# Kernel tuning notes

Hardware: AMD Instinct MI355X
Metric: run time of the kernel (lower is better)

## Reference

```python
import math
import jax, jax.numpy as jnp
import numpy as np

B, T, HIDDEN = 2, 2048, 1024
H, HKV, D = 16, 16, 64


def _rope_tables(T, D):
    inv_freq = 1.0 / (10000.0 ** (jnp.arange(0, D, 2, dtype=jnp.float32) / D))
    t = jnp.arange(T, dtype=jnp.float32)
    freqs = jnp.outer(t, inv_freq)               # [T, D/2]
    emb = jnp.concatenate([freqs, freqs], axis=-1)  # [T, D]
    return jnp.cos(emb), jnp.sin(emb)


def setup_inputs() -> dict:
    key = jax.random.key(0)
    k1, k2, k3 = jax.random.split(key, 3)
    hidden_states = jax.random.normal(k1, (B, T, HIDDEN), dtype=jnp.float32)
    cos, sin = _rope_tables(T, D)
    # trunc-normal-ish init, std = 1/sqrt(fan_in)
    w_qkv = jax.random.normal(k2, ((H + 2 * HKV) * D, HIDDEN), dtype=jnp.float32) / math.sqrt(HIDDEN)
    w_o = jax.random.normal(k3, (HIDDEN, H * D), dtype=jnp.float32) / math.sqrt(H * D)
    return {"hidden_states": hidden_states, "cos": cos, "sin": sin, "w_qkv": w_qkv, "w_o": w_o}


def _rotate_half(x):
    x1, x2 = jnp.split(x, 2, axis=-1)
    return jnp.concatenate([-x2, x1], axis=-1)


def reference(hidden_states, cos, sin, w_qkv, w_o):
    b, t, _ = hidden_states.shape
    # fused QKV projection: [B,T,(H+2*HKV)*D]
    qkv = jnp.einsum('bti,oi->bto', hidden_states, w_qkv)
    qkv = qkv.reshape(b, t, H + 2 * HKV, D)
    q = qkv[:, :, :H]                    # [B,T,H,D]
    k = qkv[:, :, H:H + HKV]             # [B,T,HKV,D]
    v = qkv[:, :, H + HKV:]              # [B,T,HKV,D]
    # inline RoPE; cos/sin broadcast over heads
    c = cos[:, None, :]
    s = sin[:, None, :]
    q = q * c + _rotate_half(q) * s
    k = k * c + _rotate_half(k) * s
    scale = 1.0 / math.sqrt(D)
    attn_scores = jnp.einsum('bthd,bThd->bhtT', q, k) * scale  # [B,H,T,T]
    mask = jnp.tril(jnp.ones((t, t), dtype=bool))
    attn_scores = jnp.where(mask[None, None, :, :], attn_scores, -1e9)
    attn = jax.nn.softmax(attn_scores, axis=-1)
    context = jnp.einsum('bhtT,bThd->bthd', attn, v).reshape(b, t, H * D)
    return jnp.einsum('bti,oi->bto', context, w_o)
```

## Files before the change

### kernel.cpp

```cpp
#include <hip/hip_runtime.h>

typedef __bf16 bf16_t;
typedef __bf16 bf16x4 __attribute__((ext_vector_type(4)));
typedef __bf16 bf16x8 __attribute__((ext_vector_type(8)));
typedef float f32x4 __attribute__((ext_vector_type(4)));
typedef unsigned int u32x2 __attribute__((ext_vector_type(2)));
typedef unsigned long long u64;

#define MFMA16(a, b, c) __builtin_amdgcn_mfma_f32_16x16x32_bf16((a), (b), (c), 0, 0, 0)

#define LDG2LDS16(g, l)                                                        \
    __builtin_amdgcn_global_load_lds(                                          \
        (const __attribute__((address_space(1))) void*)(g),                    \
        (__attribute__((address_space(3))) void*)(l), 16, 0, 0)

#if __has_builtin(__builtin_amdgcn_exp2f)
#define EXP2(x) __builtin_amdgcn_exp2f(x)
#else
#define EXP2(x) exp2f(x)
#endif

__device__ inline bf16x8 load8(const float* p) {
    const f32x4 a = *(const f32x4*)p;
    const f32x4 b = *(const f32x4*)(p + 4);
    bf16x8 r;
#pragma unroll
    for (int i = 0; i < 4; i++) { r[i] = (bf16_t)a[i]; r[4 + i] = (bf16_t)b[i]; }
    return r;
}

__device__ inline u32x2 as2(bf16x4 v) {
    u32x2 r;
    __builtin_memcpy(&r, &v, 8);
    return r;
}

__device__ inline bf16x4 shfl4(bf16x4 v, int src) {
    u64 x;
    __builtin_memcpy(&x, &v, 8);
    x = __shfl(x, src, 64);
    bf16x4 r;
    __builtin_memcpy(&r, &x, 8);
    return r;
}

__global__ __launch_bounds__(256) void convert_kernel(const float* __restrict__ hs,
                                                      const float* __restrict__ wqkv,
                                                      const float* __restrict__ wo,
                                                      bf16_t* __restrict__ outb) {
    const size_t c = ((size_t)blockIdx.x * 256 + threadIdx.x) * 8;
    const float* src;
    size_t off;
    if (c < 4194304) { src = hs; off = c; }
    else if (c < 7340032) { src = wqkv; off = c - 4194304; }
    else { src = wo; off = c - 7340032; }
    *(bf16x8*)(outb + c) = load8(src + off);
}


__global__ __launch_bounds__(512, 2) void gemm_qkv256(const bf16_t* __restrict__ A,
                                                      const bf16_t* __restrict__ B,
                                                      bf16_t* __restrict__ q_ws,
                                                      bf16_t* __restrict__ k_ws,
                                                      bf16_t* __restrict__ v_ws,
                                                      const float* __restrict__ cosb,
                                                      const float* __restrict__ sinb) {
    constexpr int K = 1024;
    __shared__ __align__(16) bf16_t As[32768];
    __shared__ __align__(16) bf16_t Bs[32768];

    const int tid = threadIdx.x;
    const int w = tid >> 6;
    const int lane = tid & 63;
    const int lr = lane & 15;
    const int quad = lane >> 4;

    const int lid = blockIdx.x;
    const int l = (lid & 7) * 24 + (lid >> 3);
    const int by = l / 12;
    const int bx = l - by * 12;
    const int m0 = by * 256;
    const int n0 = bx * 256;

    const int trow = tid >> 3;
    const int slot = (tid & 7) ^ (trow & 7);
    const bf16_t* gA = A + (size_t)(m0 + trow) * K + slot * 8;
    const bf16_t* gB = B + (size_t)(n0 + trow) * K + slot * 8;
    bf16_t* lA = As + w * 512;
    bf16_t* lB = Bs + w * 512;

    const int wmm = (w >> 2) * 128;
    const int wnn = (w & 3) * 64;
    const int offA0 = (quad ^ (lr & 7)) * 16;
    const char* Ab = (const char*)As + (wmm + lr) * 128;
    const char* Bb = (const char*)Bs + (wnn + lr) * 128;

    f32x4 acc[8][4] = {};

#define STAGE256(t, buf)                                                       \
    {                                                                          \
        _Pragma("unroll") for (int c = 0; c < 4; c++) {                        \
            LDG2LDS16(gA + (size_t)c * 65536 + (size_t)(t) * 64,               \
                      lA + (buf) * 16384 + c * 4096);                          \
            LDG2LDS16(gB + (size_t)c * 65536 + (size_t)(t) * 64,               \
                      lB + (buf) * 16384 + c * 4096);                          \
        }                                                                      \
    }

#define PHASE256(buf, qm, qn)                                                  \
    {                                                                          \
        const char* pa = Ab + (buf) * 32768 + (qm) * 8192;                     \
        const char* pb = Bb + (buf) * 32768 + (qn) * 4096;                     \
        {                                                                      \
            bf16x8 a0[4], b0[2];                                               \
            _Pragma("unroll") for (int i = 0; i < 4; i++)                      \
                a0[i] = *(const bf16x8*)(pa + i * 2048 + offA0);               \
            _Pragma("unroll") for (int jn = 0; jn < 2; jn++)                   \
                b0[jn] = *(const bf16x8*)(pb + jn * 2048 + offA0);             \
            __builtin_amdgcn_s_setprio(1);                                     \
            _Pragma("unroll") for (int i = 0; i < 4; i++)                      \
                _Pragma("unroll") for (int jn = 0; jn < 2; jn++)               \
                    acc[(qm) * 4 + i][(qn) * 2 + jn] = MFMA16(                 \
                        a0[i], b0[jn], acc[(qm) * 4 + i][(qn) * 2 + jn]);      \
            __builtin_amdgcn_s_setprio(0);                                     \
        }                                                                      \
        {                                                                      \
            bf16x8 a1[4], b1[2];                                               \
            _Pragma("unroll") for (int i = 0; i < 4; i++)                      \
                a1[i] = *(const bf16x8*)(pa + i * 2048 + (offA0 ^ 64));        \
            _Pragma("unroll") for (int jn = 0; jn < 2; jn++)                   \
                b1[jn] = *(const bf16x8*)(pb + jn * 2048 + (offA0 ^ 64));      \
            __builtin_amdgcn_s_setprio(1);                                     \
            _Pragma("unroll") for (int i = 0; i < 4; i++)                      \
                _Pragma("unroll") for (int jn = 0; jn < 2; jn++)               \
                    acc[(qm) * 4 + i][(qn) * 2 + jn] = MFMA16(                 \
                        a1[i], b1[jn], acc[(qm) * 4 + i][(qn) * 2 + jn]);      \
            __builtin_amdgcn_s_setprio(0);                                     \
        }                                                                      \
    }

    STAGE256(0, 0);
    STAGE256(1, 1);
    asm volatile("s_waitcnt vmcnt(8)" ::: "memory");
    __builtin_amdgcn_s_barrier();
    asm volatile("" ::: "memory");

#pragma unroll 2
    for (int t = 0; t < 16; t++) {
        const int buf = t & 1;
        PHASE256(buf, 0, 0);
        PHASE256(buf, 0, 1);
        PHASE256(buf, 1, 0);
        PHASE256(buf, 1, 1);
        asm volatile("s_waitcnt lgkmcnt(0)" ::: "memory");
        __builtin_amdgcn_s_barrier();
        asm volatile("" ::: "memory");
        if (t < 14) {
            STAGE256(t + 2, buf);
            asm volatile("s_waitcnt vmcnt(8)" ::: "memory");
        } else {
            asm volatile("s_waitcnt vmcnt(0)" ::: "memory");
        }
        __builtin_amdgcn_s_barrier();
        asm volatile("" ::: "memory");
    }

#undef STAGE256
#undef PHASE256

    const int j = bx * 4 + (w & 3);
    if (j < 32) {
        const bool isq = (j < 16);
        const float qs = 0.125f * 1.44269504089f;
#pragma unroll
        for (int im = 0; im < 8; im++) {
#pragma unroll
            for (int r = 0; r < 4; r++) {
                const int m = m0 + wmm + im * 16 + quad * 4 + r;
                const int b = m >> 11;
                const int t = m & 2047;
#pragma unroll
                for (int in = 0; in < 2; in++) {
                    const int d = in * 16 + lr;
                    const float x1 = acc[im][in][r];
                    const float x2 = acc[im][in + 2][r];
                    const float c = cosb[t * 64 + d];
                    const float s = sinb[t * 64 + d];
                    float y1 = x1 * c - x2 * s;
                    float y2 = x2 * c + x1 * s;
                    if (isq) {
                        y1 *= qs; y2 *= qs;
                        const size_t base =
                            ((size_t)(b * 16 + j) * 2048 + t) * 64 + d;
                        q_ws[base] = (bf16_t)y1;
                        q_ws[base + 32] = (bf16_t)y2;
                    } else {
                        const int bh = b * 16 + (j - 16);
                        const size_t off =
                            ((size_t)(bh * 128 + (t >> 4)) * 2) * 512 +
                            ((t & 15) + (d >> 3) * 16) * 8 + (d & 7);
                        k_ws[off] = (bf16_t)y1;
                        k_ws[off + 512] = (bf16_t)y2;
                    }
                }
            }
        }
    } else {
#pragma unroll
        for (int im = 0; im < 8; im++)
#pragma unroll
            for (int in = 0; in < 4; in++)
#pragma unroll
                for (int r = 0; r < 4; r++) {
                    const int m = m0 + wmm + im * 16 + quad * 4 + r;
                    const int b = m >> 11;
                    const int t = m & 2047;
                    const int d = in * 16 + lr;
                    const int bh = b * 16 + (j - 32);
                    const size_t off =
                        ((size_t)(bh * 64 + (t >> 5)) * 4 + (d >> 4)) * 512 +
                        ((d & 15) + ((t & 31) >> 3) * 16) * 8 + (t & 7);
                    v_ws[off] = (bf16_t)acc[im][in][r];
                }
    }
}

template <int MODE, int NDIM, int BM>
__global__ __launch_bounds__(256) void gemm_bt(const bf16_t* __restrict__ A,
                                               const bf16_t* __restrict__ B,
                                               float* __restrict__ outp,
                                               bf16_t* __restrict__ q_ws,
                                               bf16_t* __restrict__ k_ws,
                                               bf16_t* __restrict__ v_ws,
                                               const float* __restrict__ cosb,
                                               const float* __restrict__ sinb) {
    constexpr int K = 1024;
    constexpr int IM = BM / 32;
    __shared__ __align__(16) bf16_t As[BM * 32];
    __shared__ __align__(16) bf16_t Bs[128 * 32];

    const int tid = threadIdx.x;
    const int w = tid >> 6;
    const int lane = tid & 63;
    const int lr = lane & 15;
    const int quad = lane >> 4;
    const int m0 = blockIdx.y * BM;
    const int n0 = blockIdx.x * 128;
    const int wm = (w & 1) * (BM / 2);
    const int wn = (w >> 1) * 64;

    const int srow = tid >> 2;
    const int skk = (tid & 3) * 8;
    const bf16_t* gA0 = A + (size_t)(m0 + srow) * K + skk;
    const bf16_t* gA1 = gA0 + (size_t)64 * K;
    const bf16_t* gB0 = B + (size_t)(n0 + srow) * K + skk;
    const bf16_t* gB1 = gB0 + (size_t)64 * K;
    bf16_t* lA0 = As + w * 512;
    bf16_t* lA1 = As + 2048 + w * 512;
    bf16_t* lB0 = Bs + w * 512;
    bf16_t* lB1 = Bs + 2048 + w * 512;

    f32x4 acc[IM][4] = {};

    for (int k0 = 0; k0 < K; k0 += 32) {
        LDG2LDS16(gA0 + k0, lA0);
        if constexpr (BM == 128) LDG2LDS16(gA1 + k0, lA1);
        LDG2LDS16(gB0 + k0, lB0);
        LDG2LDS16(gB1 + k0, lB1);
        __syncthreads();

        bf16x8 af[IM], bfm[4];
#pragma unroll
        for (int im = 0; im < IM; im++)
            af[im] = *(const bf16x8*)&As[(wm + im * 16 + lr) * 32 + quad * 8];
#pragma unroll
        for (int in = 0; in < 4; in++)
            bfm[in] = *(const bf16x8*)&Bs[(wn + in * 16 + lr) * 32 + quad * 8];
#pragma unroll
        for (int im = 0; im < IM; im++)
#pragma unroll
            for (int in = 0; in < 4; in++)
                acc[im][in] = MFMA16(af[im], bfm[in], acc[im][in]);
        __syncthreads();
    }

    if constexpr (MODE == 0) {
#pragma unroll
        for (int im = 0; im < IM; im++)
#pragma unroll
            for (int in = 0; in < 4; in++)
#pragma unroll
                for (int r = 0; r < 4; r++) {
                    const int m = m0 + wm + im * 16 + quad * 4 + r;
                    const int n = n0 + wn + in * 16 + lr;
                    outp[(size_t)m * NDIM + n] = acc[im][in][r];
                }
    } else {
        const int j = (n0 + wn) >> 6;
        if (j < 32) {
            const bool isq = (j < 16);
            const float qs = 0.125f * 1.44269504089f;
#pragma unroll
            for (int im = 0; im < IM; im++) {
#pragma unroll
                for (int r = 0; r < 4; r++) {
                    const int m = m0 + wm + im * 16 + quad * 4 + r;
                    const int b = m >> 11;
                    const int t = m & 2047;
#pragma unroll
                    for (int in = 0; in < 2; in++) {
                        const int d = in * 16 + lr;
                        const float x1 = acc[im][in][r];
                        const float x2 = acc[im][in + 2][r];
                        const float c = cosb[t * 64 + d];
                        const float s = sinb[t * 64 + d];
                        float y1 = x1 * c - x2 * s;
                        float y2 = x2 * c + x1 * s;
                        if (isq) {
                            y1 *= qs; y2 *= qs;
                            const size_t base =
                                ((size_t)(b * 16 + j) * 2048 + t) * 64 + d;
                            q_ws[base] = (bf16_t)y1;
                            q_ws[base + 32] = (bf16_t)y2;
                        } else {
                            const int bh = b * 16 + (j - 16);
                            const size_t off =
                                ((size_t)(bh * 128 + (t >> 4)) * 2) * 512 +
                                ((t & 15) + (d >> 3) * 16) * 8 + (d & 7);
                            k_ws[off] = (bf16_t)y1;
                            k_ws[off + 512] = (bf16_t)y2;
                        }
                    }
                }
            }
        } else {
#pragma unroll
            for (int im = 0; im < IM; im++)
#pragma unroll
                for (int in = 0; in < 4; in++)
#pragma unroll
                    for (int r = 0; r < 4; r++) {
                        const int m = m0 + wm + im * 16 + quad * 4 + r;
                        const int b = m >> 11;
                        const int t = m & 2047;
                        const int d = in * 16 + lr;
                        const int bh = b * 16 + (j - 32);
                        const size_t off =
                            ((size_t)(bh * 64 + (t >> 5)) * 4 + (d >> 4)) * 512 +
                            ((d & 15) + ((t & 31) >> 3) * 16) * 8 + (t & 7);
                        v_ws[off] = (bf16_t)acc[im][in][r];
                    }
        }
    }
}

__device__ inline void flash_tile(int qt, int quad, int lr, int query,
                                  const bf16_t* __restrict__ kbase,
                                  const bf16_t* __restrict__ vbase,
                                  bf16x8 qlo, bf16x8 qhi,
                                  f32x4* o, float& lrun) {
    bf16x8 kc[8];
#pragma unroll
    for (int n = 0; n < 4; n++) {
        kc[2 * n] = *(const bf16x8*)(kbase + (size_t)(n * 2) * 512);
        kc[2 * n + 1] = *(const bf16x8*)(kbase + (size_t)(n * 2 + 1) * 512);
    }

    for (int kb = 0; kb <= qt; kb++) {
        bf16x8 vv[2][4];
#pragma unroll
        for (int hh = 0; hh < 2; hh++)
#pragma unroll
            for (int n = 0; n < 4; n++)
                vv[hh][n] = *(const bf16x8*)(vbase +
                    (size_t)((kb * 2 + hh) * 4 + n) * 512);

        const int kbn = (kb < qt) ? kb + 1 : kb;
        bf16x8 kn[8];
#pragma unroll
        for (int n = 0; n < 4; n++) {
            kn[2 * n] = *(const bf16x8*)(kbase + (size_t)((kbn * 4 + n) * 2) * 512);
            kn[2 * n + 1] = *(const bf16x8*)(kbase + (size_t)((kbn * 4 + n) * 2 + 1) * 512);
        }

        const int u0 = kb * 64;
        f32x4 s[4];
#pragma unroll
        for (int n = 0; n < 4; n++) {
            const f32x4 z = {};
            s[n] = MFMA16(kc[2 * n], qlo, z);
            s[n] = MFMA16(kc[2 * n + 1], qhi, s[n]);
        }

        if (kb == qt) {
#pragma unroll
            for (int n = 0; n < 4; n++)
#pragma unroll
                for (int r = 0; r < 4; r++)
                    if (u0 + n * 16 + quad * 4 + r > query) s[n][r] = -1e9f;
        }

        f32x4 p[4];
#pragma unroll
        for (int n = 0; n < 4; n++)
#pragma unroll
            for (int r = 0; r < 4; r++) p[n][r] = EXP2(s[n][r]);

        lrun += ((p[0][0] + p[0][1]) + (p[0][2] + p[0][3])) +
                ((p[1][0] + p[1][1]) + (p[1][2] + p[1][3])) +
                ((p[2][0] + p[2][1]) + (p[2][2] + p[2][3])) +
                ((p[3][0] + p[3][1]) + (p[3][2] + p[3][3]));

        bf16x4 pb[4];
#pragma unroll
        for (int n = 0; n < 4; n++)
#pragma unroll
            for (int r = 0; r < 4; r++) pb[n][r] = (bf16_t)p[n][r];

#pragma unroll
        for (int hh = 0; hh < 2; hh++) {
            bf16x8 pf;
#if __has_builtin(__builtin_amdgcn_permlane16_swap) && \
    __has_builtin(__builtin_amdgcn_permlane32_swap)
            const u32x2 P0 = as2(pb[2 * hh]);
            const u32x2 P1 = as2(pb[2 * hh + 1]);
            const u32x2 s1a = __builtin_amdgcn_permlane16_swap(P0[0], P0[1], false, false);
            const u32x2 s1b = __builtin_amdgcn_permlane16_swap(P1[0], P1[1], false, false);
            const u32x2 s2a = __builtin_amdgcn_permlane32_swap(s1a[0], s1b[0], false, false);
            const u32x2 s2b = __builtin_amdgcn_permlane32_swap(s1a[1], s1b[1], false, false);
            const u32x2 s3a = __builtin_amdgcn_permlane16_swap(s2a[0], s2a[1], false, false);
            const u32x2 s3b = __builtin_amdgcn_permlane16_swap(s2b[0], s2b[1], false, false);
            const unsigned pfd[4] = {s3a[0], s3a[1], s3b[0], s3b[1]};
            __builtin_memcpy(&pf, pfd, 16);
#else
            const int srcLow = ((quad & 1) << 5) + lr;
            const int srcHigh = srcLow + 16;
            const bool loSel = (quad < 2);
            const bf16x4 a0 = shfl4(pb[2 * hh], srcLow);
            const bf16x4 a1 = shfl4(pb[2 * hh + 1], srcLow);
            const bf16x4 b0 = shfl4(pb[2 * hh], srcHigh);
            const bf16x4 b1 = shfl4(pb[2 * hh + 1], srcHigh);
            const bf16x4 lo = loSel ? a0 : a1;
            const bf16x4 hi = loSel ? b0 : b1;
#pragma unroll
            for (int r = 0; r < 4; r++) { pf[r] = lo[r]; pf[4 + r] = hi[r]; }
#endif
#pragma unroll
            for (int n = 0; n < 4; n++)
                o[n] = MFMA16(vv[hh][n], pf, o[n]);
        }

#pragma unroll
        for (int i = 0; i < 8; i++) kc[i] = kn[i];
    }
}

__global__ __launch_bounds__(256) void attn_kernel(const bf16_t* __restrict__ q_ws,
                                                   const bf16_t* __restrict__ k_ws,
                                                   const bf16_t* __restrict__ v_ws,
                                                   bf16_t* __restrict__ ctx) {
    const int tid = threadIdx.x;
    const int w = tid >> 6;
    const int lane = tid & 63;
    const int lr = lane & 15;
    const int quad = lane >> 4;
    const int bh = blockIdx.x & 31;
    const int pr = blockIdx.x >> 5;
    const int b = bh >> 4;
    const int hd = bh & 15;

    const bf16_t* kbase = k_ws + (size_t)bh * 131072 + lane * 8;
    const bf16_t* vbase = v_ws + (size_t)bh * 131072 + lane * 8;

#pragma unroll
    for (int half = 0; half < 2; half++) {
        const int qt = half ? (31 - pr) : pr;
        const int trow = qt * 64 + w * 16;
        const int query = trow + lr;

        const bf16_t* qb = q_ws + ((size_t)bh * 2048 + trow + lr) * 64 + quad * 8;
        const bf16x8 qlo = *(const bf16x8*)qb;
        const bf16x8 qhi = *(const bf16x8*)(qb + 32);

        f32x4 o[4] = {};
        float lrun = 0.0f;
        flash_tile(qt, quad, lr, query, kbase, vbase, qlo, qhi, o, lrun);

        lrun += __shfl_xor(lrun, 16);
        lrun += __shfl_xor(lrun, 32);

        const float inv = 1.0f / fmaxf(lrun, 1e-30f);
        const size_t base = ((size_t)b * 2048 + query) * 1024 + hd * 64 + quad * 4;
#pragma unroll
        for (int n = 0; n < 4; n++) {
            bf16x4 ob;
#pragma unroll
            for (int r = 0; r < 4; r++) ob[r] = (bf16_t)(o[n][r] * inv);
            *(bf16x4*)&ctx[base + n * 16] = ob;
        }
    }
}

extern "C" void kernel_launch(void* const* d_in, const int* in_sizes, int n_in,
                              void* d_out, int out_size, void* d_ws, size_t ws_size,
                              hipStream_t stream) {
    const float* hs = (const float*)d_in[0];
    const float* cosb = (const float*)d_in[1];
    const float* sinb = (const float*)d_in[2];
    const float* wqkv = (const float*)d_in[3];
    const float* wo = (const float*)d_in[4];
    float* out = (float*)d_out;

    char* ws = (char*)d_ws;
    bf16_t* hs_b = (bf16_t*)(ws);
    bf16_t* wqkv_b = hs_b + 4194304;
    bf16_t* wo_b = hs_b + 7340032;
    bf16_t* q_ws = (bf16_t*)(ws + (size_t)(16u << 20));
    bf16_t* k_ws = (bf16_t*)(ws + (size_t)(24u << 20));
    bf16_t* v_ws = (bf16_t*)(ws + (size_t)(32u << 20));
    bf16_t* ctx = (bf16_t*)(ws);

    const dim3 blk(256);

    convert_kernel<<<dim3(4096), blk, 0, stream>>>(hs, wqkv, wo, hs_b);

    gemm_qkv256<<<dim3(192), dim3(512), 0, stream>>>(
        hs_b, wqkv_b, q_ws, k_ws, v_ws, cosb, sinb);

    attn_kernel<<<dim3(512), blk, 0, stream>>>(q_ws, k_ws, v_ws, ctx);

    gemm_bt<0, 1024, 64><<<dim3(8, 64), blk, 0, stream>>>(
        ctx, wo_b, out, nullptr, nullptr, nullptr, nullptr, nullptr);
}
```

Before: 189.0 us.

## Merge 256-tile GEMM phases into full-K slices and swizzle small GEMM LDS

The 256x256 QKV GEMM inner loop now loads all eight A fragments and four B fragments for a 32-wide K slice, then issues 32 MFMAs. This replaces four quadrant phases that each did 8 MFMAs, cutting repeated LDS reads of the same A/B fragments while raising register pressure. Separately, the smaller templated GEMM XOR-swizzles the K-column chunk on both the global-to-LDS store and the fragment read, to reduce LDS bank conflicts.

```diff
diff --git a/kernel.cpp b/kernel.cpp
--- a/kernel.cpp
+++ b/kernel.cpp
@@ -91,7 +91,7 @@
 
     const int wmm = (w >> 2) * 128;
     const int wnn = (w & 3) * 64;
-    const int offA0 = (quad ^ (lr & 7)) * 16;
+    const int sA0 = (quad ^ (lr & 7)) * 16;
     const char* Ab = (const char*)As + (wmm + lr) * 128;
     const char* Bb = (const char*)Bs + (wnn + lr) * 128;
 
@@ -107,36 +107,23 @@
         }                                                                      \
     }
 
-#define PHASE256(buf, qm, qn)                                                  \
+#define READS(buf, soff, af, bf)                                               \
     {                                                                          \
-        const char* pa = Ab + (buf) * 32768 + (qm) * 8192;                     \
-        const char* pb = Bb + (buf) * 32768 + (qn) * 4096;                     \
-        {                                                                      \
-            bf16x8 a0[4], b0[2];                                               \
-            _Pragma("unroll") for (int i = 0; i < 4; i++)                      \
-                a0[i] = *(const bf16x8*)(pa + i * 2048 + offA0);               \
-            _Pragma("unroll") for (int jn = 0; jn < 2; jn++)                   \
-                b0[jn] = *(const bf16x8*)(pb + jn * 2048 + offA0);             \
-            __builtin_amdgcn_s_setprio(1);                                     \
-            _Pragma("unroll") for (int i = 0; i < 4; i++)                      \
-                _Pragma("unroll") for (int jn = 0; jn < 2; jn++)               \
-                    acc[(qm) * 4 + i][(qn) * 2 + jn] = MFMA16(                 \
-                        a0[i], b0[jn], acc[(qm) * 4 + i][(qn) * 2 + jn]);      \
-            __builtin_amdgcn_s_setprio(0);                                     \
-        }                                                                      \
-        {                                                                      \
-            bf16x8 a1[4], b1[2];                                               \
-            _Pragma("unroll") for (int i = 0; i < 4; i++)                      \
-                a1[i] = *(const bf16x8*)(pa + i * 2048 + (offA0 ^ 64));        \
-            _Pragma("unroll") for (int jn = 0; jn < 2; jn++)                   \
-                b1[jn] = *(const bf16x8*)(pb + jn * 2048 + (offA0 ^ 64));      \
-            __builtin_amdgcn_s_setprio(1);                                     \
-            _Pragma("unroll") for (int i = 0; i < 4; i++)                      \
-                _Pragma("unroll") for (int jn = 0; jn < 2; jn++)               \
-                    acc[(qm) * 4 + i][(qn) * 2 + jn] = MFMA16(                 \
-                        a1[i], b1[jn], acc[(qm) * 4 + i][(qn) * 2 + jn]);      \
-            __builtin_amdgcn_s_setprio(0);                                     \
-        }                                                                      \
+        const char* pa = Ab + (buf) * 32768;                                   \
+        const char* pb = Bb + (buf) * 32768;                                   \
+        _Pragma("unroll") for (int im = 0; im < 8; im++)                       \
+            af[im] = *(const bf16x8*)(pa + im * 2048 + (soff));                \
+        _Pragma("unroll") for (int in = 0; in < 4; in++)                       \
+            bf[in] = *(const bf16x8*)(pb + in * 2048 + (soff));                \
+    }
+
+#define MFMAS(af, bf)                                                          \
+    {                                                                          \
+        __builtin_amdgcn_s_setprio(1);                                         \
+        _Pragma("unroll") for (int im = 0; im < 8; im++)                       \
+            _Pragma("unroll") for (int in = 0; in < 4; in++)                   \
+                acc[im][in] = MFMA16(af[im], bf[in], acc[im][in]);             \
+        __builtin_amdgcn_s_setprio(0);                                         \
     }
 
     STAGE256(0, 0);
@@ -148,10 +135,16 @@
 #pragma unroll 2
     for (int t = 0; t < 16; t++) {
         const int buf = t & 1;
-        PHASE256(buf, 0, 0);
-        PHASE256(buf, 0, 1);
-        PHASE256(buf, 1, 0);
-        PHASE256(buf, 1, 1);
+        {
+            bf16x8 a0[8], b0[4];
+            READS(buf, sA0, a0, b0);
+            MFMAS(a0, b0);
+        }
+        {
+            bf16x8 a1[8], b1[4];
+            READS(buf, sA0 ^ 64, a1, b1);
+            MFMAS(a1, b1);
+        }
         asm volatile("s_waitcnt lgkmcnt(0)" ::: "memory");
         __builtin_amdgcn_s_barrier();
         asm volatile("" ::: "memory");
@@ -166,7 +159,8 @@
     }
 
 #undef STAGE256
-#undef PHASE256
+#undef READS
+#undef MFMAS
 
     const int j = bx * 4 + (w & 3);
     if (j < 32) {
@@ -250,7 +244,7 @@
     const int wn = (w >> 1) * 64;
 
     const int srow = tid >> 2;
-    const int skk = (tid & 3) * 8;
+    const int skk = (((tid & 3) ^ ((tid >> 3) & 3)) * 8);
     const bf16_t* gA0 = A + (size_t)(m0 + srow) * K + skk;
     const bf16_t* gA1 = gA0 + (size_t)64 * K;
     const bf16_t* gB0 = B + (size_t)(n0 + srow) * K + skk;
@@ -260,6 +254,8 @@
     bf16_t* lB0 = Bs + w * 512;
     bf16_t* lB1 = Bs + 2048 + w * 512;
 
+    const int qsw = (quad ^ ((lr >> 1) & 3)) * 8;
+
     f32x4 acc[IM][4] = {};
 
     for (int k0 = 0; k0 < K; k0 += 32) {
@@ -272,10 +268,10 @@
         bf16x8 af[IM], bfm[4];
 #pragma unroll
         for (int im = 0; im < IM; im++)
-            af[im] = *(const bf16x8*)&As[(wm + im * 16 + lr) * 32 + quad * 8];
+            af[im] = *(const bf16x8*)&As[(wm + im * 16 + lr) * 32 + qsw];
 #pragma unroll
         for (int in = 0; in < 4; in++)
-            bfm[in] = *(const bf16x8*)&Bs[(wn + in * 16 + lr) * 32 + quad * 8];
+            bfm[in] = *(const bf16x8*)&Bs[(wn + in * 16 + lr) * 32 + qsw];
 #pragma unroll
         for (int im = 0; im < IM; im++)
 #pragma unroll
```

Result: no change. 187.8 us (-0.6%).
